# Optimization experiments

Measured on AMD Instinct MI355X. Metric: run time of the kernel, lower is better.

## Reference

```python
import jax, jax.numpy as jnp
import numpy as np

N, E, CIN, H, B, NCOV, NCLASS, T = 50000, 800000, 64, 64, 256, 8, 2, 3


def setup_inputs() -> dict:
    key = jax.random.key(0)
    ks = jax.random.split(key, 24)
    s = 1.0 / np.sqrt(H)
    nrm = lambda k, shp, sc: (jax.random.normal(k, shp, jnp.float32) * sc)
    p = {}
    p["x"] = nrm(ks[0], (N, 3 * CIN), 1.0)
    p["edge_index"] = jax.random.randint(ks[1], (2, E), 0, N)
    p["cov"] = nrm(ks[2], (B, NCOV), 1.0)
    p["batch"] = jnp.sort(jax.random.randint(ks[3], (N,), 0, B))
    p["h0"] = nrm(ks[4], (B, H), 1.0)
    p["c0"] = nrm(ks[5], (B, H), 1.0)
    # GCNEncoder params (shared across the 3 channel slices, as in the torch code)
    p["lin_W"] = nrm(ks[6], (CIN, H), s)
    p["lin_b"] = jnp.zeros((H,), jnp.float32)
    p["conv1_W"] = nrm(ks[7], (H, H), s)
    p["conv1_b"] = jnp.zeros((H,), jnp.float32)
    p["conv2_W"] = nrm(ks[8], (H, H), s)
    p["conv2_b"] = jnp.zeros((H,), jnp.float32)
    # LSTM (1 layer), torch gate order i,f,g,o
    p["Wih"] = nrm(ks[9], (4 * H, H), s)
    p["Whh"] = nrm(ks[10], (4 * H, H), s)
    p["bih"] = jnp.zeros((4 * H,), jnp.float32)
    p["bhh"] = jnp.zeros((4 * H,), jnp.float32)
    p["w0_W"] = nrm(ks[11], (H, H), s)
    p["w0_b"] = jnp.zeros((H,), jnp.float32)
    p["attn_W"] = nrm(ks[12], (1, H), s)
    p["attn_b"] = jnp.zeros((1,), jnp.float32)
    p["l1_W"] = nrm(ks[13], (8, H), s)
    p["l1_b"] = jnp.zeros((8,), jnp.float32)
    p["l2_W"] = nrm(ks[14], (NCLASS, 8 + NCOV), 1.0 / np.sqrt(8 + NCOV))
    p["l2_b"] = jnp.zeros((NCLASS,), jnp.float32)
    return p


def _gcn_conv(x, src, dst, dinv, W, b):
    xw = x @ W
    norm = dinv[src] * dinv[dst]                      # [E]
    agg = jax.ops.segment_sum(norm[:, None] * xw[src], dst, num_segments=N)
    agg = agg + (2.0 * dinv * dinv)[:, None] * xw     # self-loop (weight 2)
    return agg + b


def _encoder(x, src, dst, dinv, lin_W, lin_b, c1W, c1b, c2W, c2b):
    out = x @ lin_W + lin_b                           # dropout = identity (eval)
    out1 = jax.nn.relu(_gcn_conv(out, src, dst, dinv, c1W, c1b)) + out
    out2 = _gcn_conv(out1, src, dst, dinv, c2W, c2b) + out1
    return out2


def reference(x, edge_index, cov, batch, h0, c0, lin_W, lin_b, conv1_W, conv1_b,
              conv2_W, conv2_b, Wih, Whh, bih, bhh, w0_W, w0_b, attn_W, attn_b,
              l1_W, l1_b, l2_W, l2_b):
    src, dst = edge_index[0], edge_index[1]
    deg = jax.ops.segment_sum(jnp.ones((E,), jnp.float32), dst, num_segments=N) + 2.0
    dinv = jax.lax.rsqrt(deg)
    enc = lambda xi: _encoder(xi, src, dst, dinv, lin_W, lin_b,
                              conv1_W, conv1_b, conv2_W, conv2_b)
    o1 = enc(x[:, :CIN]); o2 = enc(x[:, CIN:2 * CIN]); o3 = enc(x[:, 2 * CIN:])
    # global_mean_pool per branch
    cnt = jnp.maximum(jax.ops.segment_sum(jnp.ones((N,), jnp.float32), batch,
                                          num_segments=B), 1.0)[:, None]
    pool = lambda o: jax.ops.segment_sum(o, batch, num_segments=B) / cnt
    seq = jnp.stack([pool(o1), pool(o2), pool(o3)], axis=1)  # [B, 3, H]

    # 1-layer LSTM over T=3 (torch gate order i,f,g,o)
    def step(carry, x_t):
        h, c = carry
        g = x_t @ Wih.T + bih + h @ Whh.T + bhh
        i, f, gg, o = jnp.split(g, 4, axis=-1)
        c = jax.nn.sigmoid(f) * c + jax.nn.sigmoid(i) * jnp.tanh(gg)
        h = jax.nn.sigmoid(o) * jnp.tanh(c)
        return (h, c), h

    (_, _), hs = jax.lax.scan(step, (h0, c0), jnp.swapaxes(seq, 0, 1))
    rnn_out = jnp.swapaxes(hs, 0, 1)                         # [B, T, H]
    r = jnp.tanh(rnn_out @ w0_W.T + w0_b)
    attn = jax.nn.softmax((r @ attn_W.T + attn_b)[..., 0], axis=1)  # [B, T]
    pooled = jnp.einsum('bth,bt->bh', r, attn)
    out = jax.nn.relu(pooled @ l1_W.T + l1_b)
    out = jnp.concatenate([out, cov], axis=1)
    out = out @ l2_W.T + l2_b
    return attn, out
```

## Files before the change

### kernel.cpp

```cpp
#include <hip/hip_runtime.h>
#include <math.h>


#define TT 3
#define CHUNK 2048
#define BCAP 16384

typedef __attribute__((ext_vector_type(2))) float floatx2;

__device__ __forceinline__ float sigmoidf_(float x) { return 1.f / (1.f + expf(-x)); }

__global__ void brow_sorted(const int* __restrict__ batch, int* __restrict__ brow,
                            int N, int B) {
    int n = blockIdx.x * 256 + threadIdx.x;
    if (n >= N) return;
    int b = batch[n];
    if (n == 0) {
        for (int q = 0; q <= b; ++q) brow[q] = 0;
    } else {
        int pb = batch[n - 1];
        for (int q = pb + 1; q <= b; ++q) brow[q] = n;
    }
    if (n == N - 1) {
        for (int q = b + 1; q <= B; ++q) brow[q] = N;
    }
}

__global__ void stage_direct(const int* __restrict__ src, const int* __restrict__ dst,
                             int* __restrict__ bcnt, unsigned* __restrict__ stg, int E) {
    __shared__ int hcnt[256], hbase[256], hcur[256];
    hcnt[threadIdx.x] = 0;
    __syncthreads();
    int base = blockIdx.x * CHUNK;
    for (int i = threadIdx.x; i < CHUNK; i += 256) {
        int e = base + i;
        if (e < E) atomicAdd(&hcnt[dst[e] >> 8], 1);
    }
    __syncthreads();
    int c = hcnt[threadIdx.x];
    if (c) hbase[threadIdx.x] = atomicAdd(&bcnt[threadIdx.x], c);
    hcur[threadIdx.x] = 0;
    __syncthreads();
    for (int i = threadIdx.x; i < CHUNK; i += 256) {
        int e = base + i;
        if (e < E) {
            int d = dst[e];
            int b = d >> 8;
            int r = atomicAdd(&hcur[b], 1);
            stg[(long)b * BCAP + hbase[b] + r] =
                (unsigned)src[e] | ((unsigned)(d & 255) << 24);
        }
    }
}

__global__ void scan_buckets(const int* __restrict__ bcnt, int* __restrict__ boff,
                             int nb, int E) {
    __shared__ int s[256];
    int v = (threadIdx.x < nb) ? bcnt[threadIdx.x] : 0;
    s[threadIdx.x] = v;
    __syncthreads();
    for (int off = 1; off < 256; off <<= 1) {
        int t = (threadIdx.x >= off) ? s[threadIdx.x - off] : 0;
        __syncthreads();
        s[threadIdx.x] += t;
        __syncthreads();
    }
    if (threadIdx.x < nb) boff[threadIdx.x] = s[threadIdx.x] - v;
    if (threadIdx.x == 0) boff[nb] = E;
}

__global__ void bucket_build(const unsigned* __restrict__ stg, const int* __restrict__ bcnt,
                             const int* __restrict__ boff, int* __restrict__ rowptr,
                             float* __restrict__ dinv, int* __restrict__ csrc,
                             int N, int E) {
    const int b = blockIdx.x;
    const int n0 = b << 8;
    __shared__ int cnt[256];
    __shared__ int pfx[256];
    cnt[threadIdx.x] = 0;
    __syncthreads();
    const long s = (long)b * BCAP;
    const long e = s + bcnt[b];
    for (long p = s + threadIdx.x; p < e; p += 256)
        atomicAdd(&cnt[stg[p] >> 24], 1);
    __syncthreads();
    int v = cnt[threadIdx.x];
    pfx[threadIdx.x] = v;
    __syncthreads();
    for (int off = 1; off < 256; off <<= 1) {
        int t = (threadIdx.x >= off) ? pfx[threadIdx.x - off] : 0;
        __syncthreads();
        pfx[threadIdx.x] += t;
        __syncthreads();
    }
    int rowbase = boff[b] + pfx[threadIdx.x] - v;
    int n = n0 + threadIdx.x;
    if (n < N) {
        rowptr[n] = rowbase;
        dinv[n] = rsqrtf((float)v + 2.0f);
    }
    if (b == 0 && threadIdx.x == 0) rowptr[N] = E;
    cnt[threadIdx.x] = rowbase;
    __syncthreads();
    for (long p = s + threadIdx.x; p < e; p += 256) {
        unsigned u = stg[p];
        int dl = u >> 24;
        int r = atomicAdd(&cnt[dl], 1);
        csrc[r] = (int)(u & 0xFFFFFFu);
    }
}

__global__ __launch_bounds__(256) void gemm64_f32(
    const float* __restrict__ A, int lda, long aStride,
    const float* __restrict__ W, const float* __restrict__ bias,
    float* __restrict__ C, long cStride, int nrows) {
    __shared__ float AT[64][68];
    __shared__ float Ws[64][68];
    const int t = threadIdx.x;
    const float* Ab = A + (long)blockIdx.y * aStride;
    const int r0 = blockIdx.x * 64;

    #pragma unroll
    for (int i = 0; i < 4; ++i) {
        int idx = t + i * 256;
        int k = idx >> 4, c4 = idx & 15;
        *(float4*)&Ws[k][c4 * 4] = *(const float4*)(W + k * 64 + c4 * 4);
    }
    #pragma unroll
    for (int i = 0; i < 4; ++i) {
        int idx = t + i * 256;
        int row = idx >> 4, c4 = idx & 15;
        int gr = r0 + row;
        float4 a = make_float4(0.f, 0.f, 0.f, 0.f);
        if (gr < nrows) a = *(const float4*)(Ab + (long)gr * lda + c4 * 4);
        AT[c4 * 4 + 0][row] = a.x;
        AT[c4 * 4 + 1][row] = a.y;
        AT[c4 * 4 + 2][row] = a.z;
        AT[c4 * 4 + 3][row] = a.w;
    }
    __syncthreads();

    const int rowg = t >> 4, colg = t & 15;
    float acc[4][4] = {};
    #pragma unroll 8
    for (int k = 0; k < 64; ++k) {
        float4 av = *(const float4*)&AT[k][rowg * 4];
        float4 wv = *(const float4*)&Ws[k][colg * 4];
        #pragma unroll
        for (int i = 0; i < 4; ++i) {
            acc[i][0] = fmaf(((const float*)&av)[i], wv.x, acc[i][0]);
            acc[i][1] = fmaf(((const float*)&av)[i], wv.y, acc[i][1]);
            acc[i][2] = fmaf(((const float*)&av)[i], wv.z, acc[i][2]);
            acc[i][3] = fmaf(((const float*)&av)[i], wv.w, acc[i][3]);
        }
    }
    float b0 = bias[colg * 4 + 0], b1 = bias[colg * 4 + 1];
    float b2 = bias[colg * 4 + 2], b3 = bias[colg * 4 + 3];
    float* Cb = C + (long)blockIdx.y * cStride;
    #pragma unroll
    for (int i = 0; i < 4; ++i) {
        int gr = r0 + rowg * 4 + i;
        if (gr < nrows)
            *(float4*)(Cb + (long)gr * 64 + colg * 4) =
                make_float4(acc[i][0] + b0, acc[i][1] + b1, acc[i][2] + b2, acc[i][3] + b3);
    }
}

__global__ __launch_bounds__(256) void gemm64_t8(
    const float* __restrict__ A, long aStride, const float* __restrict__ W,
    unsigned* __restrict__ T8, const float* __restrict__ dinvp, int nrows) {
    __shared__ float AT[64][68];
    __shared__ float Ws[64][68];
    const int t = threadIdx.x;
    const float* Ab = A + (long)blockIdx.y * aStride;
    const int r0 = blockIdx.x * 64;

    #pragma unroll
    for (int i = 0; i < 4; ++i) {
        int idx = t + i * 256;
        int k = idx >> 4, c4 = idx & 15;
        *(float4*)&Ws[k][c4 * 4] = *(const float4*)(W + k * 64 + c4 * 4);
    }
    #pragma unroll
    for (int i = 0; i < 4; ++i) {
        int idx = t + i * 256;
        int row = idx >> 4, c4 = idx & 15;
        int gr = r0 + row;
        float4 a = make_float4(0.f, 0.f, 0.f, 0.f);
        if (gr < nrows) a = *(const float4*)(Ab + (long)gr * 64 + c4 * 4);
        AT[c4 * 4 + 0][row] = a.x;
        AT[c4 * 4 + 1][row] = a.y;
        AT[c4 * 4 + 2][row] = a.z;
        AT[c4 * 4 + 3][row] = a.w;
    }
    __syncthreads();

    const int rowg = t >> 4, colg = t & 15;
    float acc[4][4] = {};
    #pragma unroll 8
    for (int k = 0; k < 64; ++k) {
        float4 av = *(const float4*)&AT[k][rowg * 4];
        float4 wv = *(const float4*)&Ws[k][colg * 4];
        #pragma unroll
        for (int i = 0; i < 4; ++i) {
            acc[i][0] = fmaf(((const float*)&av)[i], wv.x, acc[i][0]);
            acc[i][1] = fmaf(((const float*)&av)[i], wv.y, acc[i][1]);
            acc[i][2] = fmaf(((const float*)&av)[i], wv.z, acc[i][2]);
            acc[i][3] = fmaf(((const float*)&av)[i], wv.w, acc[i][3]);
        }
    }
    #pragma unroll
    for (int i = 0; i < 4; ++i) {
        int gr = r0 + rowg * 4 + i;
        if (gr >= nrows) continue;
        float sc = dinvp[gr];
        int r = 0;
        r = __builtin_amdgcn_cvt_pk_fp8_f32(acc[i][0] * sc, acc[i][1] * sc, r, false);
        r = __builtin_amdgcn_cvt_pk_fp8_f32(acc[i][2] * sc, acc[i][3] * sc, r, true);
        T8[(long)gr * 48 + blockIdx.y * 16 + colg] = (unsigned)r;
    }
}

#define EDGE3(uu)                                                        \
    {                                                                    \
        floatx2 lo = __builtin_amdgcn_cvt_pk_f32_fp8(uu, false);         \
        floatx2 hi = __builtin_amdgcn_cvt_pk_f32_fp8(uu, true);          \
        a0[ch] += lo.x; a1[ch] += lo.y; a2[ch] += hi.x; a3[ch] += hi.y;  \
    }

template <bool RELU>
__global__ __launch_bounds__(256) void gcn_gather3_f8(
    const int* __restrict__ rowptr, const int* __restrict__ csrc,
    const float* __restrict__ dinv, const unsigned* __restrict__ tc,
    const float* __restrict__ bias, const float* __restrict__ prev, long chS,
    float* __restrict__ outp, int N) {
    long gid = ((long)blockIdx.x * 256 + threadIdx.x) >> 4;
    int n = (int)gid;
    if (n >= N) return;
    const int jj = threadIdx.x & 15;

    const int end = rowptr[n + 1];
    const float din = dinv[n];
    float a0[TT] = {}, a1[TT] = {}, a2[TT] = {}, a3[TT] = {};
    int p = rowptr[n];
    for (; p + 7 < end; p += 8) {
        long r0 = (long)csrc[p]     * 48 + jj;
        long r1 = (long)csrc[p + 1] * 48 + jj;
        long r2 = (long)csrc[p + 2] * 48 + jj;
        long r3 = (long)csrc[p + 3] * 48 + jj;
        long r4 = (long)csrc[p + 4] * 48 + jj;
        long r5 = (long)csrc[p + 5] * 48 + jj;
        long r6 = (long)csrc[p + 6] * 48 + jj;
        long r7 = (long)csrc[p + 7] * 48 + jj;
        #pragma unroll
        for (int ch = 0; ch < TT; ++ch) {
            unsigned u0 = tc[r0 + ch * 16];
            unsigned u1 = tc[r1 + ch * 16];
            unsigned u2 = tc[r2 + ch * 16];
            unsigned u3 = tc[r3 + ch * 16];
            unsigned u4 = tc[r4 + ch * 16];
            unsigned u5 = tc[r5 + ch * 16];
            unsigned u6 = tc[r6 + ch * 16];
            unsigned u7 = tc[r7 + ch * 16];
            EDGE3(u0) EDGE3(u1) EDGE3(u2) EDGE3(u3)
            EDGE3(u4) EDGE3(u5) EDGE3(u6) EDGE3(u7)
        }
    }
    for (; p < end; ++p) {
        long r = (long)csrc[p] * 48 + jj;
        #pragma unroll
        for (int ch = 0; ch < TT; ++ch) {
            unsigned u = tc[r + ch * 16];
            EDGE3(u)
        }
    }
    float4 bv = *(const float4*)(bias + 4 * jj);
    long nrow = (long)n * 48 + jj;
    long off = (long)n * 64 + 4 * jj;
    #pragma unroll
    for (int ch = 0; ch < TT; ++ch) {
        unsigned us = tc[nrow + ch * 16];
        floatx2 slo = __builtin_amdgcn_cvt_pk_f32_fp8(us, false);
        floatx2 shi = __builtin_amdgcn_cvt_pk_f32_fp8(us, true);
        float v0 = (a0[ch] + 2.f * slo.x) * din + bv.x;
        float v1 = (a1[ch] + 2.f * slo.y) * din + bv.y;
        float v2 = (a2[ch] + 2.f * shi.x) * din + bv.z;
        float v3 = (a3[ch] + 2.f * shi.y) * din + bv.w;
        if (RELU) {
            v0 = fmaxf(v0, 0.f); v1 = fmaxf(v1, 0.f);
            v2 = fmaxf(v2, 0.f); v3 = fmaxf(v3, 0.f);
        }
        float4 pv = *(const float4*)(prev + ch * chS + off);
        *(float4*)(outp + ch * chS + off) =
            make_float4(v0 + pv.x, v1 + pv.y, v2 + pv.z, v3 + pv.w);
    }
}

__global__ __launch_bounds__(256) void pool_range(
    const float* __restrict__ out2, long chStride, const int* __restrict__ brow,
    float* __restrict__ seq) {
    const int b = blockIdx.x;
    const int chan = blockIdx.y;
    const float* src = out2 + (long)chan * chStride;
    const int j = threadIdx.x & 63;
    const int w = threadIdx.x >> 6;
    __shared__ float part[4][64];
    float acc = 0.f;
    const int s = brow[b], e = brow[b + 1];
    for (int n = s + w; n < e; n += 4) acc += src[(long)n * 64 + j];
    part[w][j] = acc;
    __syncthreads();
    if (w == 0)
        seq[((long)b * TT + chan) * 64 + j] = part[0][j] + part[1][j] + part[2][j] + part[3][j];
}

__global__ __launch_bounds__(256) void head_kernel(
    const float* __restrict__ seq, const int* __restrict__ brow,
    const float* __restrict__ h0, const float* __restrict__ c0,
    const float* __restrict__ Wih, const float* __restrict__ Whh,
    const float* __restrict__ bih, const float* __restrict__ bhh,
    const float* __restrict__ w0W, const float* __restrict__ w0b,
    const float* __restrict__ attnW, const float* __restrict__ attnb,
    const float* __restrict__ l1W, const float* __restrict__ l1b,
    const float* __restrict__ l2W, const float* __restrict__ l2b,
    const float* __restrict__ cov, float* __restrict__ out_attn,
    float* __restrict__ out_cls) {
    const int b = blockIdx.x;
    const int t = threadIdx.x;

    __shared__ float x[TT][64];
    __shared__ float h[64], c[64];
    __shared__ float gates[256];
    __shared__ float rnn[TT][64];
    __shared__ float r[TT][64];
    __shared__ float logit[TT];
    __shared__ float a[TT];
    __shared__ float pooled[64];
    __shared__ float l1o[16];

    float inv = 1.0f / fmaxf((float)(brow[b + 1] - brow[b]), 1.0f);
    if (t < TT * 64) x[t / 64][t % 64] = seq[(long)b * TT * 64 + t] * inv;
    if (t < 64) { h[t] = h0[(long)b * 64 + t]; c[t] = c0[(long)b * 64 + t]; }
    __syncthreads();

    for (int step = 0; step < TT; ++step) {
        float g = bih[t] + bhh[t];
        const float* wi = Wih + (long)t * 64;
        const float* wh = Whh + (long)t * 64;
        #pragma unroll 8
        for (int k = 0; k < 64; ++k) g += wi[k] * x[step][k] + wh[k] * h[k];
        gates[t] = g;
        __syncthreads();
        if (t < 64) {
            float ig = sigmoidf_(gates[t]);
            float fg = sigmoidf_(gates[64 + t]);
            float gg = tanhf(gates[128 + t]);
            float og = sigmoidf_(gates[192 + t]);
            float cn = fg * c[t] + ig * gg;
            c[t] = cn;
            float hn = og * tanhf(cn);
            h[t] = hn;
            rnn[step][t] = hn;
        }
        __syncthreads();
    }

    if (t < TT * 64) {
        int tt = t / 64, j = t % 64;
        float v = w0b[j];
        const float* wr = w0W + (long)j * 64;
        #pragma unroll 8
        for (int k = 0; k < 64; ++k) v += rnn[tt][k] * wr[k];
        r[tt][j] = tanhf(v);
    }
    __syncthreads();

    if (t < TT) {
        float v = attnb[0];
        #pragma unroll 8
        for (int k = 0; k < 64; ++k) v += r[t][k] * attnW[k];
        logit[t] = v;
    }
    __syncthreads();

    if (t == 0) {
        float m = fmaxf(logit[0], fmaxf(logit[1], logit[2]));
        float e0 = expf(logit[0] - m), e1 = expf(logit[1] - m), e2 = expf(logit[2] - m);
        float s = e0 + e1 + e2;
        a[0] = e0 / s; a[1] = e1 / s; a[2] = e2 / s;
        out_attn[(long)b * TT + 0] = a[0];
        out_attn[(long)b * TT + 1] = a[1];
        out_attn[(long)b * TT + 2] = a[2];
    }
    __syncthreads();

    if (t < 64) pooled[t] = a[0] * r[0][t] + a[1] * r[1][t] + a[2] * r[2][t];
    __syncthreads();

    if (t < 8) {
        float v = l1b[t];
        const float* w = l1W + (long)t * 64;
        #pragma unroll 8
        for (int k = 0; k < 64; ++k) v += pooled[k] * w[k];
        l1o[t] = fmaxf(v, 0.f);
    } else if (t < 16) {
        l1o[t] = cov[(long)b * 8 + (t - 8)];
    }
    __syncthreads();

    if (t < 2) {
        float v = l2b[t];
        const float* w = l2W + (long)t * 16;
        #pragma unroll
        for (int k = 0; k < 16; ++k) v += l1o[k] * w[k];
        out_cls[(long)b * 2 + t] = v;
    }
}

extern "C" void kernel_launch(void* const* d_in, const int* in_sizes, int n_in,
                              void* d_out, int out_size, void* d_ws, size_t ws_size,
                              hipStream_t stream) {
    const float* x       = (const float*)d_in[0];
    const int*   eidx    = (const int*)d_in[1];
    const float* cov     = (const float*)d_in[2];
    const int*   batch   = (const int*)d_in[3];
    const float* h0      = (const float*)d_in[4];
    const float* c0      = (const float*)d_in[5];
    const float* lin_W   = (const float*)d_in[6];
    const float* lin_b   = (const float*)d_in[7];
    const float* conv1_W = (const float*)d_in[8];
    const float* conv1_b = (const float*)d_in[9];
    const float* conv2_W = (const float*)d_in[10];
    const float* conv2_b = (const float*)d_in[11];
    const float* Wih     = (const float*)d_in[12];
    const float* Whh     = (const float*)d_in[13];
    const float* bih     = (const float*)d_in[14];
    const float* bhh     = (const float*)d_in[15];
    const float* w0_W    = (const float*)d_in[16];
    const float* w0_b    = (const float*)d_in[17];
    const float* attn_W  = (const float*)d_in[18];
    const float* attn_b  = (const float*)d_in[19];
    const float* l1_W    = (const float*)d_in[20];
    const float* l1_b    = (const float*)d_in[21];
    const float* l2_W    = (const float*)d_in[22];
    const float* l2_b    = (const float*)d_in[23];

    const int N = in_sizes[3];
    const int E = in_sizes[1] / 2;
    const int B = in_sizes[2] / 8;

    const int* src = eidx;
    const int* dst = eidx + E;

    auto cdiv = [](long a, long b) { return (int)((a + b - 1) / b); };
    const int nb = cdiv(N, 256);

    char* w = (char*)d_ws;
    float* dinv   = (float*)w;  w += (size_t)N * 4;
    int*   rowptr = (int*)w;    w += (size_t)(N + 1) * 4;
    int*   brow   = (int*)w;    w += (size_t)(B + 1) * 4;
    int*   bcnt   = (int*)w;    w += 256 * 4;
    int*   boff   = (int*)w;    w += 260 * 4;
    int*   csrc   = (int*)w;    w += (size_t)E * 4;
    unsigned* stg = (unsigned*)w; w += (size_t)nb * BCAP * 4;
    float* seq    = (float*)w;  w += (size_t)B * TT * 64 * 4;
    float* buf0   = (float*)w;  w += (size_t)TT * N * 64 * 4;
    float* bufA   = (float*)w;  w += (size_t)TT * N * 64 * 4;
    unsigned* tb8 = (unsigned*)w;  w += (size_t)N * 48 * 4;
    const long chS = (long)N * 64;

    float* out_attn = (float*)d_out;
    float* out_cls  = out_attn + (long)B * TT;

    hipMemsetAsync(bcnt, 0, 256 * 4, stream);
    brow_sorted<<<cdiv(N, 256), 256, 0, stream>>>(batch, brow, N, B);
    stage_direct<<<cdiv(E, CHUNK), 256, 0, stream>>>(src, dst, bcnt, stg, E);
    scan_buckets<<<1, 256, 0, stream>>>(bcnt, boff, nb, E);
    bucket_build<<<nb, 256, 0, stream>>>(stg, bcnt, boff, rowptr, dinv, csrc, N, E);

    const int gemm_gx = cdiv(N, 64);
    const int ng_gx   = cdiv((long)N * 16, 256);

    {
        dim3 ggrid(gemm_gx, TT);
        gemm64_f32<<<ggrid, 256, 0, stream>>>(x, 3 * 64, 64, lin_W, lin_b,
                                              buf0, chS, N);
    }
    {
        dim3 ggrid(gemm_gx, TT);
        gemm64_t8<<<ggrid, 256, 0, stream>>>(buf0, chS, conv1_W, tb8, dinv, N);
    }
    gcn_gather3_f8<true><<<ng_gx, 256, 0, stream>>>(
        rowptr, csrc, dinv, tb8, conv1_b, buf0, chS, bufA, N);
    {
        dim3 ggrid(gemm_gx, TT);
        gemm64_t8<<<ggrid, 256, 0, stream>>>(bufA, chS, conv2_W, tb8, dinv, N);
    }
    gcn_gather3_f8<false><<<ng_gx, 256, 0, stream>>>(
        rowptr, csrc, dinv, tb8, conv2_b, bufA, chS, buf0, N);

    {
        dim3 pgrid(B, TT);
        pool_range<<<pgrid, 256, 0, stream>>>(buf0, chS, brow, seq);
    }

    head_kernel<<<B, 256, 0, stream>>>(seq, brow, h0, c0, Wih, Whh, bih, bhh,
                                       w0_W, w0_b, attn_W, attn_b, l1_W, l1_b,
                                       l2_W, l2_b, cov, out_attn, out_cls);
}
```

Measured before the change: 248.5 us.

## Sort nodes by degree within each bucket to balance gather wavefronts

The bucket build now also counting-sorts the 256 nodes of each bucket by in-degree and writes a node order. Invalid padding nodes are keyed last and map to ids at or above N, which return early. Both GCN gather kernels process nodes in that order, so the 4 nodes sharing a 64-lane wavefront have similar edge counts and less lane divergence. The gather inner unroll also drops from 8 to 4 edges. This adds an extra shared histogram and scan in bucket_build plus an indirection load, and gives up some memory-level parallelism per node.

```diff
diff --git a/kernel.cpp b/kernel.cpp
--- a/kernel.cpp
+++ b/kernel.cpp
@@ -72,11 +72,12 @@
 __global__ void bucket_build(const unsigned* __restrict__ stg, const int* __restrict__ bcnt,
                              const int* __restrict__ boff, int* __restrict__ rowptr,
                              float* __restrict__ dinv, int* __restrict__ csrc,
-                             int N, int E) {
+                             int* __restrict__ nodeorder, int N, int E) {
     const int b = blockIdx.x;
     const int n0 = b << 8;
     __shared__ int cnt[256];
     __shared__ int pfx[256];
+    __shared__ int dh[256];
     cnt[threadIdx.x] = 0;
     __syncthreads();
     const long s = (long)b * BCAP;
@@ -84,7 +85,7 @@
     for (long p = s + threadIdx.x; p < e; p += 256)
         atomicAdd(&cnt[stg[p] >> 24], 1);
     __syncthreads();
-    int v = cnt[threadIdx.x];
+    const int v = cnt[threadIdx.x];
     pfx[threadIdx.x] = v;
     __syncthreads();
     for (int off = 1; off < 256; off <<= 1) {
@@ -93,13 +94,34 @@
         pfx[threadIdx.x] += t;
         __syncthreads();
     }
-    int rowbase = boff[b] + pfx[threadIdx.x] - v;
-    int n = n0 + threadIdx.x;
-    if (n < N) {
+    const int rowbase = boff[b] + pfx[threadIdx.x] - v;
+    const int n = n0 + threadIdx.x;
+    const bool valid = (n < N);
+    if (valid) {
         rowptr[n] = rowbase;
         dinv[n] = rsqrtf((float)v + 2.0f);
     }
     if (b == 0 && threadIdx.x == 0) rowptr[N] = E;
+
+    const int key = valid ? min(v, 255) : 255;
+    dh[threadIdx.x] = 0;
+    __syncthreads();
+    atomicAdd(&dh[key], 1);
+    __syncthreads();
+    int dv = dh[threadIdx.x];
+    pfx[threadIdx.x] = dv;
+    __syncthreads();
+    for (int off = 1; off < 256; off <<= 1) {
+        int t = (threadIdx.x >= off) ? pfx[threadIdx.x - off] : 0;
+        __syncthreads();
+        pfx[threadIdx.x] += t;
+        __syncthreads();
+    }
+    dh[threadIdx.x] = pfx[threadIdx.x] - dv;
+    __syncthreads();
+    int rank = atomicAdd(&dh[key], 1);
+    nodeorder[n0 + rank] = n;
+
     cnt[threadIdx.x] = rowbase;
     __syncthreads();
     for (long p = s + threadIdx.x; p < e; p += 256) {
@@ -231,11 +253,12 @@
 template <bool RELU>
 __global__ __launch_bounds__(256) void gcn_gather3_f8(
     const int* __restrict__ rowptr, const int* __restrict__ csrc,
+    const int* __restrict__ nodeorder,
     const float* __restrict__ dinv, const unsigned* __restrict__ tc,
     const float* __restrict__ bias, const float* __restrict__ prev, long chS,
     float* __restrict__ outp, int N) {
     long gid = ((long)blockIdx.x * 256 + threadIdx.x) >> 4;
-    int n = (int)gid;
+    int n = nodeorder[gid];
     if (n >= N) return;
     const int jj = threadIdx.x & 15;
 
@@ -243,27 +266,18 @@
     const float din = dinv[n];
     float a0[TT] = {}, a1[TT] = {}, a2[TT] = {}, a3[TT] = {};
     int p = rowptr[n];
-    for (; p + 7 < end; p += 8) {
+    for (; p + 3 < end; p += 4) {
         long r0 = (long)csrc[p]     * 48 + jj;
         long r1 = (long)csrc[p + 1] * 48 + jj;
         long r2 = (long)csrc[p + 2] * 48 + jj;
         long r3 = (long)csrc[p + 3] * 48 + jj;
-        long r4 = (long)csrc[p + 4] * 48 + jj;
-        long r5 = (long)csrc[p + 5] * 48 + jj;
-        long r6 = (long)csrc[p + 6] * 48 + jj;
-        long r7 = (long)csrc[p + 7] * 48 + jj;
         #pragma unroll
         for (int ch = 0; ch < TT; ++ch) {
             unsigned u0 = tc[r0 + ch * 16];
             unsigned u1 = tc[r1 + ch * 16];
             unsigned u2 = tc[r2 + ch * 16];
             unsigned u3 = tc[r3 + ch * 16];
-            unsigned u4 = tc[r4 + ch * 16];
-            unsigned u5 = tc[r5 + ch * 16];
-            unsigned u6 = tc[r6 + ch * 16];
-            unsigned u7 = tc[r7 + ch * 16];
             EDGE3(u0) EDGE3(u1) EDGE3(u2) EDGE3(u3)
-            EDGE3(u4) EDGE3(u5) EDGE3(u6) EDGE3(u7)
         }
     }
     for (; p < end; ++p) {
@@ -461,6 +475,7 @@
     int*   brow   = (int*)w;    w += (size_t)(B + 1) * 4;
     int*   bcnt   = (int*)w;    w += 256 * 4;
     int*   boff   = (int*)w;    w += 260 * 4;
+    int*   nodeo  = (int*)w;    w += (size_t)nb * 256 * 4;
     int*   csrc   = (int*)w;    w += (size_t)E * 4;
     unsigned* stg = (unsigned*)w; w += (size_t)nb * BCAP * 4;
     float* seq    = (float*)w;  w += (size_t)B * TT * 64 * 4;
@@ -476,10 +491,11 @@
     brow_sorted<<<cdiv(N, 256), 256, 0, stream>>>(batch, brow, N, B);
     stage_direct<<<cdiv(E, CHUNK), 256, 0, stream>>>(src, dst, bcnt, stg, E);
     scan_buckets<<<1, 256, 0, stream>>>(bcnt, boff, nb, E);
-    bucket_build<<<nb, 256, 0, stream>>>(stg, bcnt, boff, rowptr, dinv, csrc, N, E);
+    bucket_build<<<nb, 256, 0, stream>>>(stg, bcnt, boff, rowptr, dinv, csrc,
+                                         nodeo, N, E);
 
     const int gemm_gx = cdiv(N, 64);
-    const int ng_gx   = cdiv((long)N * 16, 256);
+    const int ng_gx   = nb * 16;
 
     {
         dim3 ggrid(gemm_gx, TT);
@@ -491,13 +507,13 @@
         gemm64_t8<<<ggrid, 256, 0, stream>>>(buf0, chS, conv1_W, tb8, dinv, N);
     }
     gcn_gather3_f8<true><<<ng_gx, 256, 0, stream>>>(
-        rowptr, csrc, dinv, tb8, conv1_b, buf0, chS, bufA, N);
+        rowptr, csrc, nodeo, dinv, tb8, conv1_b, buf0, chS, bufA, N);
     {
         dim3 ggrid(gemm_gx, TT);
         gemm64_t8<<<ggrid, 256, 0, stream>>>(bufA, chS, conv2_W, tb8, dinv, N);
     }
     gcn_gather3_f8<false><<<ng_gx, 256, 0, stream>>>(
-        rowptr, csrc, dinv, tb8, conv2_b, bufA, chS, buf0, N);
+        rowptr, csrc, nodeo, dinv, tb8, conv2_b, bufA, chS, buf0, N);
 
     {
         dim3 pgrid(B, TT);
```

Result: slower. 264.4 us (+6.4%).
